# Kernel tuning notes

Hardware: AMD Instinct MI355X
Metric: run time of the kernel (lower is better)

## Reference

```python
import jax, jax.numpy as jnp
import numpy as np

NUM_HEADS = 8
OUT_FEATS = 128
D_HEAD = OUT_FEATS // NUM_HEADS
N_NODES = 50000
N_EDGES = 600000
IN_FEATS = 128


def setup_inputs() -> dict:
    key = jax.random.key(0)
    ks = jax.random.split(key, 10)
    h = jax.random.normal(ks[0], (N_NODES, IN_FEATS), dtype=jnp.float32)
    src = jax.random.randint(ks[1], (N_EDGES,), 0, N_NODES)
    dst = jax.random.randint(ks[2], (N_EDGES,), 0, N_NODES)
    s = 1.0 / np.sqrt(IN_FEATS)
    W_Q = jax.random.normal(ks[3], (IN_FEATS, OUT_FEATS), dtype=jnp.float32) * s
    W_K = jax.random.normal(ks[4], (IN_FEATS, OUT_FEATS), dtype=jnp.float32) * s
    W_V = jax.random.normal(ks[5], (IN_FEATS, OUT_FEATS), dtype=jnp.float32) * s
    b_Q = jnp.zeros((OUT_FEATS,), dtype=jnp.float32)
    b_K = jnp.zeros((OUT_FEATS,), dtype=jnp.float32)
    b_V = jnp.zeros((OUT_FEATS,), dtype=jnp.float32)
    return {"h": h, "W_Q": W_Q, "b_Q": b_Q, "W_K": W_K, "b_K": b_K,
            "W_V": W_V, "b_V": b_V, "src": src, "dst": dst}


def _graph_conv(h, W, b, src, dst, norm_src, norm_dst):
    # DGL GraphConv, norm='both': D_dst^{-1/2} * A * D_src^{-1/2} * (h W) + b
    x = (h * norm_src[:, None]) @ W                              # [N, F]
    agg = jax.ops.segment_sum(x[src], dst, num_segments=h.shape[0])
    return agg * norm_dst[:, None] + b


def reference(h, W_Q, b_Q, W_K, b_K, W_V, b_V, src, dst):
    N = h.shape[0]
    ones = jnp.ones(src.shape[0], dtype=h.dtype)
    deg_out = jax.ops.segment_sum(ones, src, num_segments=N)   # out-degree (src side)
    deg_in = jax.ops.segment_sum(ones, dst, num_segments=N)    # in-degree (dst side)
    norm_src = jax.lax.rsqrt(jnp.clip(deg_out, 1.0))
    norm_dst = jax.lax.rsqrt(jnp.clip(deg_in, 1.0))

    Q = jax.nn.relu(_graph_conv(h, W_Q, b_Q, src, dst, norm_src, norm_dst))
    K = jax.nn.relu(_graph_conv(h, W_K, b_K, src, dst, norm_src, norm_dst))
    V = jax.nn.relu(_graph_conv(h, W_V, b_V, src, dst, norm_src, norm_dst))

    Qh = Q.reshape(N, NUM_HEADS, D_HEAD)
    Kh = K.reshape(N, NUM_HEADS, D_HEAD)
    Vh = V.reshape(N, NUM_HEADS, D_HEAD)

    # edge-wise scores: K at src dotted with Q at dst, per head
    score = jnp.sum(Kh[src] * Qh[dst], axis=-1, keepdims=True)   # [E, H, 1]
    score = jnp.exp(jnp.clip(score / np.sqrt(D_HEAD), -10.0, 10.0))

    wV = jax.ops.segment_sum(Vh[src] * score, dst, num_segments=N)  # [N, H, Dh]
    z = jax.ops.segment_sum(score, dst, num_segments=N)             # [N, H, 1]
    return wV / (z + 1e-6)
```

## Files before the change

### kernel.cpp

```cpp
#include <hip/hip_runtime.h>

#define INF  128
#define OUTF 128
#define NH   8
#define DHD  16
#define CAP  48

typedef __attribute__((ext_vector_type(8))) short bf16x8;
typedef __attribute__((ext_vector_type(4))) float f32x4;

__device__ __forceinline__ float bf16_to_f32(unsigned short u) {
    union { unsigned int i; float f; } v;
    v.i = ((unsigned int)u) << 16;
    return v.f;
}
__device__ __forceinline__ unsigned short f32_to_bf16(float f) {
    union { float f; unsigned int i; } v;
    v.f = f;
    unsigned int x = v.i;
    return (unsigned short)((x + 0x7fffu + ((x >> 16) & 1u)) >> 16);
}

__global__ void k_front(const int* __restrict__ src, const int* __restrict__ dst,
                        int* __restrict__ deg_out, int* __restrict__ cursor,
                        int* __restrict__ edge_src, int E, int SB, int HB,
                        const float* __restrict__ h, unsigned short* __restrict__ h_b, int N,
                        const float* __restrict__ Wq, const float* __restrict__ Wk,
                        const float* __restrict__ Wv, unsigned short* __restrict__ frag) {
    if (blockIdx.x < (unsigned)SB) {
        int t = blockIdx.x * 256 + threadIdx.x;
        if (t < E) {
            int s = src[t];
            int d = dst[t];
            atomicAdd(&deg_out[s], 1);
            int p = atomicAdd(&cursor[d], 1);
            if (p < CAP) edge_src[d * CAP + p] = s;
        }
    } else if (blockIdx.x < (unsigned)(SB + HB)) {
        int t = (blockIdx.x - SB) * 256 + threadIdx.x;
        if (t < N * (INF / 8)) {
            const float4* p = reinterpret_cast<const float4*>(h + (size_t)t * 8);
            float4 v0 = p[0], v1 = p[1];
            uint4 o;
            o.x = (unsigned int)f32_to_bf16(v0.x) | ((unsigned int)f32_to_bf16(v0.y) << 16);
            o.y = (unsigned int)f32_to_bf16(v0.z) | ((unsigned int)f32_to_bf16(v0.w) << 16);
            o.z = (unsigned int)f32_to_bf16(v1.x) | ((unsigned int)f32_to_bf16(v1.y) << 16);
            o.w = (unsigned int)f32_to_bf16(v1.z) | ((unsigned int)f32_to_bf16(v1.w) << 16);
            *reinterpret_cast<uint4*>(h_b + (size_t)t * 8) = o;
        }
    } else {
        int t = (blockIdx.x - SB - HB) * 256 + threadIdx.x;
        if (t >= 3 * 8 * 4 * 2 * 64) return;
        int lane  = t & 63;
        int plane = (t >> 6) & 1;
        int ks    = (t >> 7) & 3;
        int nt    = (t >> 9) & 7;
        int mat   = t >> 12;
        const float* W = (mat == 0) ? Wq : ((mat == 1) ? Wk : Wv);
        int ln = lane & 15, quad = lane >> 4;
        int n = nt * 16 + ln;
        unsigned short vals[8];
        #pragma unroll
        for (int j = 0; j < 8; ++j) {
            int k = ks * 32 + quad * 8 + j;
            float a = W[k * OUTF + n];
            unsigned short hb = f32_to_bf16(a);
            vals[j] = plane ? f32_to_bf16(a - bf16_to_f32(hb)) : hb;
        }
        unsigned int* dp = reinterpret_cast<unsigned int*>(frag + (size_t)t * 8);
        #pragma unroll
        for (int j = 0; j < 4; ++j)
            dp[j] = (unsigned int)vals[2 * j] | ((unsigned int)vals[2 * j + 1] << 16);
    }
}

__global__ __launch_bounds__(256) void k_aggemm(const unsigned short* __restrict__ h_b,
                                                const int* __restrict__ deg_out,
                                                const int* __restrict__ cursor,
                                                const int* __restrict__ edge_src,
                                                const unsigned short* __restrict__ frag,
                                                const float* __restrict__ bq,
                                                const float* __restrict__ bk,
                                                const float* __restrict__ bv,
                                                float* __restrict__ qbuf,
                                                unsigned short* __restrict__ kvbuf,
                                                int N) {
    int wave = threadIdx.x >> 6;
    int lane = threadIdx.x & 63;
    int ln   = lane & 15;
    int quad = lane >> 4;
    int mrow = blockIdx.x * 64 + wave * 16;
    int node = mrow + ln;

    float acc_a[4][8];
    #pragma unroll
    for (int ks = 0; ks < 4; ++ks)
        #pragma unroll
        for (int j = 0; j < 8; ++j) acc_a[ks][j] = 0.f;

    int deg = 0;
    const int* rowp = edge_src + (size_t)node * CAP;
    if (node < N) { deg = cursor[node]; if (deg > CAP) deg = CAP; }

    auto proc = [&](int e) {
        int s = rowp[e];
        int dg = deg_out[s]; if (dg < 1) dg = 1;
        float ns = rsqrtf((float)dg);
        const unsigned short* hrow = h_b + (size_t)s * INF + quad * 8;
        #pragma unroll
        for (int ks = 0; ks < 4; ++ks) {
            uint4 v = *reinterpret_cast<const uint4*>(hrow + ks * 32);
            acc_a[ks][0] += ns * bf16_to_f32((unsigned short)(v.x & 0xffffu));
            acc_a[ks][1] += ns * bf16_to_f32((unsigned short)(v.x >> 16));
            acc_a[ks][2] += ns * bf16_to_f32((unsigned short)(v.y & 0xffffu));
            acc_a[ks][3] += ns * bf16_to_f32((unsigned short)(v.y >> 16));
            acc_a[ks][4] += ns * bf16_to_f32((unsigned short)(v.z & 0xffffu));
            acc_a[ks][5] += ns * bf16_to_f32((unsigned short)(v.z >> 16));
            acc_a[ks][6] += ns * bf16_to_f32((unsigned short)(v.w & 0xffffu));
            acc_a[ks][7] += ns * bf16_to_f32((unsigned short)(v.w >> 16));
        }
    };
    int e = 0;
    for (; e + 2 <= deg; e += 2) { proc(e); proc(e + 1); }
    if (e < deg) proc(e);

    bf16x8 ah[4], al[4];
    #pragma unroll
    for (int ks = 0; ks < 4; ++ks)
        #pragma unroll
        for (int j = 0; j < 8; ++j) {
            unsigned short hb = f32_to_bf16(acc_a[ks][j]);
            ah[ks][j] = (short)hb;
            al[ks][j] = (short)f32_to_bf16(acc_a[ks][j] - bf16_to_f32(hb));
        }

    float nrm[4];
    #pragma unroll
    for (int r = 0; r < 4; ++r) {
        int m = mrow + quad * 4 + r;
        if (m < N) {
            int dg = cursor[m]; if (dg < 1) dg = 1;
            nrm[r] = rsqrtf((float)dg);
        } else nrm[r] = 0.f;
    }

    #pragma unroll
    for (int mat = 0; mat < 3; ++mat) {
        const float* bb = (mat == 0) ? bq : ((mat == 1) ? bk : bv);
        #pragma unroll 2
        for (int nt = 0; nt < 8; ++nt) {
            f32x4 acc = {0.f, 0.f, 0.f, 0.f};
            #pragma unroll
            for (int ks = 0; ks < 4; ++ks) {
                size_t base = ((size_t)(((mat * 8 + nt) * 4 + ks) * 2) * 64 + lane) * 8;
                bf16x8 bh = *reinterpret_cast<const bf16x8*>(frag + base);
                bf16x8 bl = *reinterpret_cast<const bf16x8*>(frag + base + 64 * 8);
                acc = __builtin_amdgcn_mfma_f32_16x16x32_bf16(ah[ks], bh, acc, 0, 0, 0);
                acc = __builtin_amdgcn_mfma_f32_16x16x32_bf16(al[ks], bh, acc, 0, 0, 0);
                acc = __builtin_amdgcn_mfma_f32_16x16x32_bf16(ah[ks], bl, acc, 0, 0, 0);
            }
            int col = nt * 16 + ln;
            float bias = bb[col];
            #pragma unroll
            for (int r = 0; r < 4; ++r) {
                int m = mrow + quad * 4 + r;
                if (m < N) {
                    float v = acc[r] * nrm[r] + bias;
                    v = (v > 0.f) ? v : 0.f;
                    if (mat == 0) {
                        qbuf[(size_t)m * OUTF + col] = v;
                    } else {
                        int idx = ((col >> 2) << 3) + (col & 3) + ((mat == 2) ? 4 : 0);
                        kvbuf[(size_t)m * 2 * OUTF + idx] = f32_to_bf16(v);
                    }
                }
            }
        }
    }
}

__global__ __launch_bounds__(256) void k_attn(const float* __restrict__ qbuf,
                                              const unsigned short* __restrict__ kvbuf,
                                              const int* __restrict__ cursor,
                                              const int* __restrict__ edge_src,
                                              float* __restrict__ out, int N) {
    int wid  = (blockIdx.x * 256 + threadIdx.x) >> 6;
    int lane = threadIdx.x & 63;
    if (wid >= N) return;
    int half = lane >> 5, li = lane & 31;
    int c4 = li * 4;
    float4 q = *reinterpret_cast<const float4*>(qbuf + (size_t)wid * OUTF + c4);
    float a0 = 0.f, a1 = 0.f, a2 = 0.f, a3 = 0.f, z = 0.f;
    int deg = cursor[wid]; if (deg > CAP) deg = CAP;
    const int* row = edge_src + wid * CAP;
    auto proc = [&](int e) {
        int s = row[e];
        uint4 kp = *reinterpret_cast<const uint4*>(kvbuf + (size_t)s * 2 * OUTF + li * 8);
        float p = q.x * bf16_to_f32((unsigned short)(kp.x & 0xffffu))
                + q.y * bf16_to_f32((unsigned short)(kp.x >> 16))
                + q.z * bf16_to_f32((unsigned short)(kp.y & 0xffffu))
                + q.w * bf16_to_f32((unsigned short)(kp.y >> 16));
        p += __shfl_xor(p, 1);
        p += __shfl_xor(p, 2);
        float w = __expf(fminf(fmaxf(0.25f * p, -10.f), 10.f));
        z  += w;
        a0 += w * bf16_to_f32((unsigned short)(kp.z & 0xffffu));
        a1 += w * bf16_to_f32((unsigned short)(kp.z >> 16));
        a2 += w * bf16_to_f32((unsigned short)(kp.w & 0xffffu));
        a3 += w * bf16_to_f32((unsigned short)(kp.w >> 16));
    };
    int e = half;
    for (; e + 4 <= deg; e += 4) { proc(e); proc(e + 2); }
    for (; e < deg; e += 2) proc(e);
    a0 += __shfl_xor(a0, 32);
    a1 += __shfl_xor(a1, 32);
    a2 += __shfl_xor(a2, 32);
    a3 += __shfl_xor(a3, 32);
    z  += __shfl_xor(z, 32);
    if (half == 0) {
        float inv = 1.0f / (z + 1e-6f);
        *reinterpret_cast<float4*>(out + (size_t)wid * OUTF + c4) =
            make_float4(a0 * inv, a1 * inv, a2 * inv, a3 * inv);
    }
}

extern "C" void kernel_launch(void* const* d_in, const int* in_sizes, int n_in,
                              void* d_out, int out_size, void* d_ws, size_t ws_size,
                              hipStream_t stream) {
    const float* h  = (const float*)d_in[0];
    const float* Wq = (const float*)d_in[1];
    const float* bq = (const float*)d_in[2];
    const float* Wk = (const float*)d_in[3];
    const float* bk = (const float*)d_in[4];
    const float* Wv = (const float*)d_in[5];
    const float* bv = (const float*)d_in[6];
    const int* src = (const int*)d_in[7];
    const int* dst = (const int*)d_in[8];

    const int N = in_sizes[0] / INF;
    const int E = in_sizes[7];

    char* ws = (char*)d_ws;
    size_t off = 0;
    auto carve = [&](size_t bytes) -> void* {
        void* p = ws + off;
        off = (off + bytes + 255) & ~(size_t)255;
        return p;
    };
    int*   zeroed    = (int*)  carve((size_t)2 * N * sizeof(int));
    int*   deg_out   = zeroed;
    int*   cursor    = zeroed + N;
    int*   edge_src  = (int*)  carve((size_t)N * CAP * sizeof(int));
    unsigned short* h_b  = (unsigned short*)carve((size_t)N * INF * sizeof(unsigned short));
    float* qbuf      = (float*)carve((size_t)N * OUTF * sizeof(float));
    unsigned short* kvbuf = (unsigned short*)carve((size_t)N * 2 * OUTF * sizeof(unsigned short));
    unsigned short* wfrag = (unsigned short*)carve((size_t)3 * 8 * 4 * 2 * 64 * 8 * sizeof(unsigned short));
    (void)ws_size;

    float* out = (float*)d_out;

    hipMemsetAsync(zeroed, 0, (size_t)2 * N * sizeof(int), stream);

    int SB = (E + 255) / 256;
    int HB = (N * (INF / 8) + 255) / 256;
    int WB = (3 * 8 * 4 * 2 * 64 + 255) / 256;
    k_front<<<SB + HB + WB, 256, 0, stream>>>(src, dst, deg_out, cursor, edge_src,
                                              E, SB, HB, h, h_b, N, Wq, Wk, Wv, wfrag);

    int gFuse = (N + 63) / 64;
    k_aggemm<<<gFuse, 256, 0, stream>>>(h_b, deg_out, cursor, edge_src, wfrag,
                                        bq, bk, bv, qbuf, kvbuf, N);

    int gAttn = (N + 3) / 4;
    k_attn<<<gAttn, 256, 0, stream>>>(qbuf, kvbuf, cursor, edge_src, out, N);
}
```

Measured before the change: 257.8 us.

## Split aggregation and GEMM across wave pairs with LDS exchange

Each 16-node tile is now handled by two waves instead of one. Each wave gathers half of the 128 input features for the tile and writes its partial accumulators to shared memory, then reads the other wave's half after a barrier. Each wave then computes half of the output column tiles. This doubles the number of waves working on the gather and GEMM, which adds parallelism and memory-level concurrency. The cost is an LDS exchange, a block-wide barrier, and each neighbour's index and degree being loaded twice.

```diff
diff --git a/kernel.cpp b/kernel.cpp
--- a/kernel.cpp
+++ b/kernel.cpp
@@ -5,6 +5,7 @@
 #define NH   8
 #define DHD  16
 #define CAP  48
+#define XPAD 20
 
 typedef __attribute__((ext_vector_type(8))) short bf16x8;
 typedef __attribute__((ext_vector_type(4))) float f32x4;
@@ -85,18 +86,21 @@
                                                 float* __restrict__ qbuf,
                                                 unsigned short* __restrict__ kvbuf,
                                                 int N) {
+    __shared__ float xch[2][2][64][XPAD];
     int wave = threadIdx.x >> 6;
     int lane = threadIdx.x & 63;
+    int pair = wave >> 1;
+    int sub  = wave & 1;
     int ln   = lane & 15;
     int quad = lane >> 4;
-    int mrow = blockIdx.x * 64 + wave * 16;
+    int mrow = blockIdx.x * 32 + pair * 16;
     int node = mrow + ln;
 
-    float acc_a[4][8];
+    float acc_h[2][8];
     #pragma unroll
-    for (int ks = 0; ks < 4; ++ks)
-        #pragma unroll
-        for (int j = 0; j < 8; ++j) acc_a[ks][j] = 0.f;
+    for (int kk = 0; kk < 2; ++kk)
+        #pragma unroll
+        for (int j = 0; j < 8; ++j) acc_h[kk][j] = 0.f;
 
     int deg = 0;
     const int* rowp = edge_src + (size_t)node * CAP;
@@ -106,23 +110,45 @@
         int s = rowp[e];
         int dg = deg_out[s]; if (dg < 1) dg = 1;
         float ns = rsqrtf((float)dg);
-        const unsigned short* hrow = h_b + (size_t)s * INF + quad * 8;
-        #pragma unroll
-        for (int ks = 0; ks < 4; ++ks) {
-            uint4 v = *reinterpret_cast<const uint4*>(hrow + ks * 32);
-            acc_a[ks][0] += ns * bf16_to_f32((unsigned short)(v.x & 0xffffu));
-            acc_a[ks][1] += ns * bf16_to_f32((unsigned short)(v.x >> 16));
-            acc_a[ks][2] += ns * bf16_to_f32((unsigned short)(v.y & 0xffffu));
-            acc_a[ks][3] += ns * bf16_to_f32((unsigned short)(v.y >> 16));
-            acc_a[ks][4] += ns * bf16_to_f32((unsigned short)(v.z & 0xffffu));
-            acc_a[ks][5] += ns * bf16_to_f32((unsigned short)(v.z >> 16));
-            acc_a[ks][6] += ns * bf16_to_f32((unsigned short)(v.w & 0xffffu));
-            acc_a[ks][7] += ns * bf16_to_f32((unsigned short)(v.w >> 16));
+        const unsigned short* hrow = h_b + (size_t)s * INF + quad * 8 + sub * 64;
+        #pragma unroll
+        for (int kk = 0; kk < 2; ++kk) {
+            uint4 v = *reinterpret_cast<const uint4*>(hrow + kk * 32);
+            acc_h[kk][0] += ns * bf16_to_f32((unsigned short)(v.x & 0xffffu));
+            acc_h[kk][1] += ns * bf16_to_f32((unsigned short)(v.x >> 16));
+            acc_h[kk][2] += ns * bf16_to_f32((unsigned short)(v.y & 0xffffu));
+            acc_h[kk][3] += ns * bf16_to_f32((unsigned short)(v.y >> 16));
+            acc_h[kk][4] += ns * bf16_to_f32((unsigned short)(v.z & 0xffffu));
+            acc_h[kk][5] += ns * bf16_to_f32((unsigned short)(v.z >> 16));
+            acc_h[kk][6] += ns * bf16_to_f32((unsigned short)(v.w & 0xffffu));
+            acc_h[kk][7] += ns * bf16_to_f32((unsigned short)(v.w >> 16));
         }
     };
     int e = 0;
     for (; e + 2 <= deg; e += 2) { proc(e); proc(e + 1); }
     if (e < deg) proc(e);
+
+    {
+        float* w = &xch[pair][sub][lane][0];
+        *reinterpret_cast<float4*>(w + 0)  = make_float4(acc_h[0][0], acc_h[0][1], acc_h[0][2], acc_h[0][3]);
+        *reinterpret_cast<float4*>(w + 4)  = make_float4(acc_h[0][4], acc_h[0][5], acc_h[0][6], acc_h[0][7]);
+        *reinterpret_cast<float4*>(w + 8)  = make_float4(acc_h[1][0], acc_h[1][1], acc_h[1][2], acc_h[1][3]);
+        *reinterpret_cast<float4*>(w + 12) = make_float4(acc_h[1][4], acc_h[1][5], acc_h[1][6], acc_h[1][7]);
+    }
+    __syncthreads();
+    float acc_a[4][8];
+    {
+        const float* rdp = &xch[pair][sub ^ 1][lane][0];
+        #pragma unroll
+        for (int kk = 0; kk < 2; ++kk) {
+            int ks_own = sub * 2 + kk, ks_oth = (sub ^ 1) * 2 + kk;
+            #pragma unroll
+            for (int j = 0; j < 8; ++j) {
+                acc_a[ks_own][j] = acc_h[kk][j];
+                acc_a[ks_oth][j] = rdp[kk * 8 + j];
+            }
+        }
+    }
 
     bf16x8 ah[4], al[4];
     #pragma unroll
@@ -148,7 +174,8 @@
     for (int mat = 0; mat < 3; ++mat) {
         const float* bb = (mat == 0) ? bq : ((mat == 1) ? bk : bv);
         #pragma unroll 2
-        for (int nt = 0; nt < 8; ++nt) {
+        for (int nth = 0; nth < 4; ++nth) {
+            int nt = sub * 4 + nth;
             f32x4 acc = {0.f, 0.f, 0.f, 0.f};
             #pragma unroll
             for (int ks = 0; ks < 4; ++ks) {
@@ -267,7 +294,7 @@
     k_front<<<SB + HB + WB, 256, 0, stream>>>(src, dst, deg_out, cursor, edge_src,
                                               E, SB, HB, h, h_b, N, Wq, Wk, Wv, wfrag);
 
-    int gFuse = (N + 63) / 64;
+    int gFuse = (N + 31) / 32;
     k_aggemm<<<gFuse, 256, 0, stream>>>(h_b, deg_out, cursor, edge_src, wfrag,
                                         bq, bk, bv, qbuf, kvbuf, N);
 
```

Result: slower. 277.3 us (+7.6%).
